# Kernel optimization log

Hardware: AMD Instinct MI355X
Metric: run time of the kernel (lower is better)

## Reference

```python
import jax, jax.numpy as jnp
import numpy as np

D_K = 64  # per-head dim; source hardcodes d_k for the 1/sqrt(d_k) scale


def setup_inputs() -> dict:
    key = jax.random.key(0)
    kq, kk, kv = jax.random.split(key, 3)
    shape = (4, 16, 2048, D_K)  # [B, H, S, d]
    return {
        "q_s": jax.random.normal(kq, shape, dtype=jnp.float32),
        "k_s": jax.random.normal(kk, shape, dtype=jnp.float32),
        "v_s": jax.random.normal(kv, shape, dtype=jnp.float32),
    }


def reference(q_s, k_s, v_s):
    # scores = Q K^T / sqrt(d_k)  -> [B, H, S, S] (full matrix, unfused, as in source)
    scale = 1.0 / jnp.sqrt(jnp.asarray(D_K, dtype=q_s.dtype))
    scores = jnp.einsum("bhqd,bhkd->bhqk", q_s, k_s) * scale
    attn = jax.nn.softmax(scores, axis=-1)
    # out = attn @ V -> [B, H, S, d]
    return jnp.einsum("bhqk,bhkd->bhqd", attn, v_s)
```

## Files before the change

kernel.cpp:

```cpp
#include <hip/hip_runtime.h>
#include <stdint.h>
#include <math.h>

#define S_LEN 2048
#define DIM   64
#define QBLK  128
#define KVBLK 64
#define NKV   (S_LEN / KVBLK)

typedef __attribute__((ext_vector_type(8))) short short8;
typedef __attribute__((ext_vector_type(4))) float f32x4;

static __device__ __forceinline__ unsigned short f2bf(float f) {
    union { float f; uint32_t u; } cv; cv.f = f;
    uint32_t u = cv.u;
    return (unsigned short)((u + 0x7fffu + ((u >> 16) & 1u)) >> 16);
}

static __device__ __forceinline__ void gload16(const void* g, void* l) {
    __builtin_amdgcn_global_load_lds(
        (const __attribute__((address_space(1))) unsigned int*)g,
        (__attribute__((address_space(3))) unsigned int*)l, 16, 0, 0);
}

static __device__ __forceinline__ float vmax3(float a, float b, float c) {
    float d;
    asm("v_max3_f32 %0, %1, %2, %3" : "=v"(d) : "v"(a), "v"(b), "v"(c));
    return d;
}

__global__ void cvt_k(const float* __restrict__ kp, unsigned short* __restrict__ kws) {
    const int idx = blockIdx.x * 256 + threadIdx.x;
    const int c   = idx & 7;
    const int s   = (idx >> 3) & (S_LEN - 1);
    const int bh  = idx >> 14;
    const float* src = kp + ((size_t)bh * S_LEN + s) * DIM + c * 8;
    const f32x4 a = *reinterpret_cast<const f32x4*>(src);
    const f32x4 b = *reinterpret_cast<const f32x4*>(src + 4);
    short8 t;
    t[0] = (short)f2bf(a[0]); t[1] = (short)f2bf(a[1]);
    t[2] = (short)f2bf(a[2]); t[3] = (short)f2bf(a[3]);
    t[4] = (short)f2bf(b[0]); t[5] = (short)f2bf(b[1]);
    t[6] = (short)f2bf(b[2]); t[7] = (short)f2bf(b[3]);
    unsigned short* dst = kws + ((size_t)bh * S_LEN + s) * DIM + (size_t)((c ^ (s & 7)) * 8);
    *reinterpret_cast<short8*>(dst) = t;
}

__global__ void cvt_v(const float* __restrict__ vp, unsigned short* __restrict__ vtws) {
    const int bh = blockIdx.x >> 5;
    const int t  = blockIdx.x & 31;
    const int tid = threadIdx.x;
    __shared__ unsigned short ldsT[DIM][72];

    const int i = tid >> 2;
    const int dbase = (tid & 3) * 16;
    const float* src = vp + ((size_t)bh * S_LEN + t * 64 + i) * DIM + dbase;
#pragma unroll
    for (int q4 = 0; q4 < 4; ++q4) {
        const f32x4 a = *reinterpret_cast<const f32x4*>(src + q4 * 4);
#pragma unroll
        for (int j = 0; j < 4; ++j) ldsT[dbase + q4 * 4 + j][i] = f2bf(a[j]);
    }
    __syncthreads();
#pragma unroll
    for (int hh = 0; hh < 2; ++hh) {
        const int slot = tid + hh * 256;
        const int d = slot >> 3, c_st = slot & 7;
        const int cl = c_st ^ (d & 7);
        short8 t8;
#pragma unroll
        for (int j = 0; j < 8; ++j) {
            const int p = cl * 8 + j;
            const int kap = (p & 32) | ((p & 16) >> 1) | ((p & 8) >> 1) | ((p & 4) << 2) | (p & 3);
            t8[j] = (short)ldsT[d][kap];
        }
        unsigned short* dst = vtws + ((size_t)bh * DIM + d) * S_LEN + t * 64 + c_st * 8;
        *reinterpret_cast<short8*>(dst) = t8;
    }
}

__global__ __launch_bounds__(256, 4)
void attn_fwd(const float* __restrict__ qp, const unsigned short* __restrict__ kws,
              const unsigned short* __restrict__ vtws, float* __restrict__ op) {
    const int lb = (blockIdx.x & 7) * 128 + (blockIdx.x >> 3);
    const int bh = lb >> 4;
    const int qb = lb & 15;
    const int tid  = threadIdx.x;
    const int wave = tid >> 6;
    const int lane = tid & 63;
    const int g = lane >> 4;
    const int r = lane & 15;

    __shared__ unsigned short klds[2][KVBLK * DIM];
    __shared__ unsigned short vlds[2][DIM * KVBLK];

    const float*          qg    = qp   + (size_t)bh * (S_LEN * DIM);
    const unsigned short* kbase = kws  + (size_t)bh * (S_LEN * DIM);
    const unsigned short* vbase = vtws + (size_t)bh * (S_LEN * DIM);
    float*                og    = op   + (size_t)bh * (S_LEN * DIM);

    const float qscale = 0.125f * 1.44269504088896340736f;
    const int q0 = qb * QBLK + wave * 32;
    short8 qfrag[2][2];
#pragma unroll
    for (int mt = 0; mt < 2; ++mt) {
        const float* qrow = qg + (size_t)(q0 + mt * 16 + r) * DIM;
#pragma unroll
        for (int ks = 0; ks < 2; ++ks) {
            const f32x4 a = *reinterpret_cast<const f32x4*>(qrow + ks * 32 + 8 * g);
            const f32x4 b = *reinterpret_cast<const f32x4*>(qrow + ks * 32 + 8 * g + 4);
            short8 t;
            t[0] = (short)f2bf(a[0] * qscale); t[1] = (short)f2bf(a[1] * qscale);
            t[2] = (short)f2bf(a[2] * qscale); t[3] = (short)f2bf(a[3] * qscale);
            t[4] = (short)f2bf(b[0] * qscale); t[5] = (short)f2bf(b[1] * qscale);
            t[6] = (short)f2bf(b[2] * qscale); t[7] = (short)f2bf(b[3] * qscale);
            qfrag[mt][ks] = t;
        }
    }

    int off[4][2];
#pragma unroll
    for (int nt = 0; nt < 4; ++nt)
#pragma unroll
        for (int ks = 0; ks < 2; ++ks)
            off[nt][ks] = (nt * 16 + r) * DIM + (((ks << 2) | g) ^ (r & 7)) * 8;

    f32x4 o[2][4];
    float m_run[2], l_part[2];
#pragma unroll
    for (int mt = 0; mt < 2; ++mt) {
#pragma unroll
        for (int nt = 0; nt < 4; ++nt) { f32x4 z = {0.f, 0.f, 0.f, 0.f}; o[mt][nt] = z; }
        m_run[mt] = -INFINITY; l_part[mt] = 0.0f;
    }

    const int srow = lane >> 3, schk = lane & 7;
    auto stage = [&](int t, int buf) {
        const int kv0 = t * KVBLK;
#pragma unroll
        for (int h = 0; h < 2; ++h) {
            const int row = wave * 16 + h * 8;
            gload16(kbase + (size_t)(kv0 + row + srow) * DIM + schk * 8,
                    &klds[buf][row * DIM]);
            gload16(vbase + (size_t)(row + srow) * S_LEN + kv0 + schk * 8,
                    &vlds[buf][row * DIM]);
        }
    };

    stage(0, 0);
    __syncthreads();
    int cur = 0;

    const f32x4 z4 = {0.f, 0.f, 0.f, 0.f};

    for (int t = 0; t < NKV; ++t) {
        if (t + 1 < NKV) stage(t + 1, cur ^ 1);

        const unsigned short* kl = &klds[cur][0];
        const unsigned short* vl = &vlds[cur][0];

        f32x4 st[2][4];
        __builtin_amdgcn_s_setprio(1);
#pragma unroll
        for (int nt = 0; nt < 4; ++nt) {
            const short8 kf0 = *reinterpret_cast<const short8*>(kl + off[nt][0]);
            const short8 kf1 = *reinterpret_cast<const short8*>(kl + off[nt][1]);
            st[0][nt] = __builtin_amdgcn_mfma_f32_16x16x32_bf16(kf0, qfrag[0][0], z4, 0, 0, 0);
            st[1][nt] = __builtin_amdgcn_mfma_f32_16x16x32_bf16(kf0, qfrag[1][0], z4, 0, 0, 0);
            st[0][nt] = __builtin_amdgcn_mfma_f32_16x16x32_bf16(kf1, qfrag[0][1], st[0][nt], 0, 0, 0);
            st[1][nt] = __builtin_amdgcn_mfma_f32_16x16x32_bf16(kf1, qfrag[1][1], st[1][nt], 0, 0, 0);
        }
        __builtin_amdgcn_s_setprio(0);

#pragma unroll
        for (int mt = 0; mt < 2; ++mt) {
            const f32x4 s0 = st[mt][0], s1 = st[mt][1], s2 = st[mt][2], s3 = st[mt][3];
            const float a0 = vmax3(s0[0], s0[1], s0[2]);
            const float a1 = vmax3(s0[3], s1[0], s1[1]);
            const float a2 = vmax3(s1[2], s1[3], s2[0]);
            const float a3 = vmax3(s2[1], s2[2], s2[3]);
            const float a4 = vmax3(s3[0], s3[1], s3[2]);
            const float lane_mx = fmaxf(vmax3(a0, a1, a2), vmax3(a3, a4, s3[3]));
            if (__any(lane_mx > m_run[mt] + 8.0f)) {
                float mx = fmaxf(lane_mx, __shfl_xor(lane_mx, 16));
                mx = fmaxf(mx, __shfl_xor(mx, 32));
                const float mnew = fmaxf(m_run[mt], mx);
                const float al = __builtin_amdgcn_exp2f(m_run[mt] - mnew);
                m_run[mt] = mnew;
                l_part[mt] *= al;
#pragma unroll
                for (int nt = 0; nt < 4; ++nt) {
                    f32x4 tt = o[mt][nt];
                    tt[0] *= al; tt[1] *= al; tt[2] *= al; tt[3] *= al;
                    o[mt][nt] = tt;
                }
            }
            const float mnow = m_run[mt];
            f32x4 p[4];
#pragma unroll
            for (int nt = 0; nt < 4; ++nt) {
                p[nt][0] = __builtin_amdgcn_exp2f(st[mt][nt][0] - mnow);
                p[nt][1] = __builtin_amdgcn_exp2f(st[mt][nt][1] - mnow);
                p[nt][2] = __builtin_amdgcn_exp2f(st[mt][nt][2] - mnow);
                p[nt][3] = __builtin_amdgcn_exp2f(st[mt][nt][3] - mnow);
            }
            l_part[mt] += ((p[0][0] + p[0][1]) + (p[0][2] + p[0][3]))
                        + ((p[1][0] + p[1][1]) + (p[1][2] + p[1][3]))
                        + ((p[2][0] + p[2][1]) + (p[2][2] + p[2][3]))
                        + ((p[3][0] + p[3][1]) + (p[3][2] + p[3][3]));
            short8 pfrag[2];
#pragma unroll
            for (int ks = 0; ks < 2; ++ks) {
                union { uint32_t u[4]; short8 v; } fr;
                asm("v_cvt_pk_bf16_f32 %0, %1, %2" : "=v"(fr.u[0])
                    : "v"(p[2*ks][0]),   "v"(p[2*ks][1]));
                asm("v_cvt_pk_bf16_f32 %0, %1, %2" : "=v"(fr.u[1])
                    : "v"(p[2*ks][2]),   "v"(p[2*ks][3]));
                asm("v_cvt_pk_bf16_f32 %0, %1, %2" : "=v"(fr.u[2])
                    : "v"(p[2*ks+1][0]), "v"(p[2*ks+1][1]));
                asm("v_cvt_pk_bf16_f32 %0, %1, %2" : "=v"(fr.u[3])
                    : "v"(p[2*ks+1][2]), "v"(p[2*ks+1][3]));
                pfrag[ks] = fr.v;
            }
            __builtin_amdgcn_s_setprio(1);
#pragma unroll
            for (int ntd = 0; ntd < 4; ++ntd) {
                const short8 vf0 = *reinterpret_cast<const short8*>(vl + off[ntd][0]);
                const short8 vf1 = *reinterpret_cast<const short8*>(vl + off[ntd][1]);
                o[mt][ntd] = __builtin_amdgcn_mfma_f32_16x16x32_bf16(vf0, pfrag[0], o[mt][ntd], 0, 0, 0);
                o[mt][ntd] = __builtin_amdgcn_mfma_f32_16x16x32_bf16(vf1, pfrag[1], o[mt][ntd], 0, 0, 0);
            }
            __builtin_amdgcn_s_setprio(0);
        }

        __syncthreads();
        cur ^= 1;
    }

#pragma unroll
    for (int mt = 0; mt < 2; ++mt) {
        float lfull = l_part[mt];
        lfull += __shfl_xor(lfull, 16);
        lfull += __shfl_xor(lfull, 32);
        const float inv = 1.0f / lfull;
        float* dst = og + (size_t)(q0 + mt * 16 + r) * DIM + 4 * g;
#pragma unroll
        for (int ntd = 0; ntd < 4; ++ntd) {
            f32x4 tt = o[mt][ntd];
            tt[0] *= inv; tt[1] *= inv; tt[2] *= inv; tt[3] *= inv;
            *reinterpret_cast<f32x4*>(dst + ntd * 16) = tt;
        }
    }
}

extern "C" void kernel_launch(void* const* d_in, const int* in_sizes, int n_in,
                              void* d_out, int out_size, void* d_ws, size_t ws_size,
                              hipStream_t stream) {
    const float* q = (const float*)d_in[0];
    const float* k = (const float*)d_in[1];
    const float* v = (const float*)d_in[2];
    float* out = (float*)d_out;
    unsigned short* kws  = (unsigned short*)d_ws;
    unsigned short* vtws = kws + (size_t)64 * S_LEN * DIM;
    cvt_k<<<dim3(64 * S_LEN * 8 / 256), 256, 0, stream>>>(k, kws);
    cvt_v<<<dim3(64 * (S_LEN / 64)), 256, 0, stream>>>(v, vtws);
    attn_fwd<<<dim3(1024), 256, 0, stream>>>(q, kws, vtws, out);
}
```

Measured before the change: 110.3 us.

## Software-pipeline QK^T of the next KV tile with softmax and PV of the current tile

Splits K and V staging and restructures the KV loop so the QK^T MFMAs for tile t+1 are issued alongside the softmax and PV work for tile t. Two score register sets are used in ping-pong, and the loop is unrolled by two to keep buffer indices static. K is staged one tile ahead, while V for the current tile is staged during the same step. The goal is to overlap exp/VALU softmax work with matrix-core work. The cost is roughly 32 more accumulator VGPRs per lane, which could reduce occupancy, and the setprio hints around QK^T are dropped.

```diff
diff --git a/kernel.cpp b/kernel.cpp
--- a/kernel.cpp
+++ b/kernel.cpp
@@ -135,46 +135,43 @@
     }
 
     const int srow = lane >> 3, schk = lane & 7;
-    auto stage = [&](int t, int buf) {
+    auto stageK = [&](int t, int buf) {
         const int kv0 = t * KVBLK;
 #pragma unroll
         for (int h = 0; h < 2; ++h) {
             const int row = wave * 16 + h * 8;
             gload16(kbase + (size_t)(kv0 + row + srow) * DIM + schk * 8,
                     &klds[buf][row * DIM]);
+        }
+    };
+    auto stageV = [&](int t, int buf) {
+        const int kv0 = t * KVBLK;
+#pragma unroll
+        for (int h = 0; h < 2; ++h) {
+            const int row = wave * 16 + h * 8;
             gload16(vbase + (size_t)(row + srow) * S_LEN + kv0 + schk * 8,
                     &vlds[buf][row * DIM]);
         }
     };
 
-    stage(0, 0);
-    __syncthreads();
-    int cur = 0;
-
     const f32x4 z4 = {0.f, 0.f, 0.f, 0.f};
 
-    for (int t = 0; t < NKV; ++t) {
-        if (t + 1 < NKV) stage(t + 1, cur ^ 1);
-
-        const unsigned short* kl = &klds[cur][0];
-        const unsigned short* vl = &vlds[cur][0];
-
-        f32x4 st[2][4];
-        __builtin_amdgcn_s_setprio(1);
+    auto qk = [&](f32x4 (&stC)[2][4], const unsigned short* kl) {
 #pragma unroll
         for (int nt = 0; nt < 4; ++nt) {
             const short8 kf0 = *reinterpret_cast<const short8*>(kl + off[nt][0]);
             const short8 kf1 = *reinterpret_cast<const short8*>(kl + off[nt][1]);
-            st[0][nt] = __builtin_amdgcn_mfma_f32_16x16x32_bf16(kf0, qfrag[0][0], z4, 0, 0, 0);
-            st[1][nt] = __builtin_amdgcn_mfma_f32_16x16x32_bf16(kf0, qfrag[1][0], z4, 0, 0, 0);
-            st[0][nt] = __builtin_amdgcn_mfma_f32_16x16x32_bf16(kf1, qfrag[0][1], st[0][nt], 0, 0, 0);
-            st[1][nt] = __builtin_amdgcn_mfma_f32_16x16x32_bf16(kf1, qfrag[1][1], st[1][nt], 0, 0, 0);
-        }
-        __builtin_amdgcn_s_setprio(0);
-
+            stC[0][nt] = __builtin_amdgcn_mfma_f32_16x16x32_bf16(kf0, qfrag[0][0], z4, 0, 0, 0);
+            stC[1][nt] = __builtin_amdgcn_mfma_f32_16x16x32_bf16(kf0, qfrag[1][0], z4, 0, 0, 0);
+            stC[0][nt] = __builtin_amdgcn_mfma_f32_16x16x32_bf16(kf1, qfrag[0][1], stC[0][nt], 0, 0, 0);
+            stC[1][nt] = __builtin_amdgcn_mfma_f32_16x16x32_bf16(kf1, qfrag[1][1], stC[1][nt], 0, 0, 0);
+        }
+    };
+
+    auto smpv = [&](f32x4 (&stP)[2][4], const unsigned short* vl) {
 #pragma unroll
         for (int mt = 0; mt < 2; ++mt) {
-            const f32x4 s0 = st[mt][0], s1 = st[mt][1], s2 = st[mt][2], s3 = st[mt][3];
+            const f32x4 s0 = stP[mt][0], s1 = stP[mt][1], s2 = stP[mt][2], s3 = stP[mt][3];
             const float a0 = vmax3(s0[0], s0[1], s0[2]);
             const float a1 = vmax3(s0[3], s1[0], s1[1]);
             const float a2 = vmax3(s1[2], s1[3], s2[0]);
@@ -199,10 +196,10 @@
             f32x4 p[4];
 #pragma unroll
             for (int nt = 0; nt < 4; ++nt) {
-                p[nt][0] = __builtin_amdgcn_exp2f(st[mt][nt][0] - mnow);
-                p[nt][1] = __builtin_amdgcn_exp2f(st[mt][nt][1] - mnow);
-                p[nt][2] = __builtin_amdgcn_exp2f(st[mt][nt][2] - mnow);
-                p[nt][3] = __builtin_amdgcn_exp2f(st[mt][nt][3] - mnow);
+                p[nt][0] = __builtin_amdgcn_exp2f(stP[mt][nt][0] - mnow);
+                p[nt][1] = __builtin_amdgcn_exp2f(stP[mt][nt][1] - mnow);
+                p[nt][2] = __builtin_amdgcn_exp2f(stP[mt][nt][2] - mnow);
+                p[nt][3] = __builtin_amdgcn_exp2f(stP[mt][nt][3] - mnow);
             }
             l_part[mt] += ((p[0][0] + p[0][1]) + (p[0][2] + p[0][3]))
                         + ((p[1][0] + p[1][1]) + (p[1][2] + p[1][3]))
@@ -232,10 +229,35 @@
             }
             __builtin_amdgcn_s_setprio(0);
         }
-
-        __syncthreads();
-        cur ^= 1;
-    }
+    };
+
+    f32x4 stA[2][4], stB[2][4];
+
+    stageK(0, 0); stageV(0, 0);
+    __syncthreads();
+    stageK(1, 1);
+    qk(stA, &klds[0][0]);
+    __syncthreads();
+
+    for (int tt = 1; tt < NKV; tt += 2) {
+        {
+            const int t = tt;
+            if (t + 1 < NKV) stageK(t + 1, 0);
+            stageV(t, 1);
+            qk(stB, &klds[1][0]);
+            smpv(stA, &vlds[0][0]);
+            __syncthreads();
+        }
+        if (tt + 1 < NKV) {
+            const int t = tt + 1;
+            stageK(t + 1, 1);
+            stageV(t, 0);
+            qk(stA, &klds[0][0]);
+            smpv(stB, &vlds[1][0]);
+            __syncthreads();
+        }
+    }
+    smpv(stB, &vlds[1][0]);
 
 #pragma unroll
     for (int mt = 0; mt < 2; ++mt) {
```

Result: slower. 274.1 us (+148.5%).

## Halve Q and KV tiles, stage V through registers into padded LDS

Applied to the files above, without the earlier changes.

The Q block drops from 128 to 64 rows, so each wave now owns 16 query rows instead of 32. The KV block drops from 64 to 32, the grid doubles to 2048 blocks, and launch bounds target 8 blocks per CU for higher occupancy. V tiles are no longer copied straight into LDS. They are loaded into registers and written into an LDS buffer padded to a row stride of 40 after compute, and the loader addresses the column chunks of the existing V layout. In exchange, each K/V tile is reused by half as many query rows, so global and L2 traffic per output roughly doubles, and there are twice as many barriers per row.

```diff
diff --git a/kernel.cpp b/kernel.cpp
--- a/kernel.cpp
+++ b/kernel.cpp
@@ -4,9 +4,10 @@
 
 #define S_LEN 2048
 #define DIM   64
-#define QBLK  128
-#define KVBLK 64
+#define QBLK  64
+#define KVBLK 32
 #define NKV   (S_LEN / KVBLK)
+#define VSTR  40
 
 typedef __attribute__((ext_vector_type(8))) short short8;
 typedef __attribute__((ext_vector_type(4))) float f32x4;
@@ -79,12 +80,12 @@
     }
 }
 
-__global__ __launch_bounds__(256, 4)
+__global__ __launch_bounds__(256, 8)
 void attn_fwd(const float* __restrict__ qp, const unsigned short* __restrict__ kws,
               const unsigned short* __restrict__ vtws, float* __restrict__ op) {
-    const int lb = (blockIdx.x & 7) * 128 + (blockIdx.x >> 3);
-    const int bh = lb >> 4;
-    const int qb = lb & 15;
+    const int lb = (blockIdx.x & 7) * 256 + (blockIdx.x >> 3);
+    const int bh = lb >> 5;
+    const int qb = lb & 31;
     const int tid  = threadIdx.x;
     const int wave = tid >> 6;
     const int lane = tid & 63;
@@ -92,7 +93,7 @@
     const int r = lane & 15;
 
     __shared__ unsigned short klds[2][KVBLK * DIM];
-    __shared__ unsigned short vlds[2][DIM * KVBLK];
+    __shared__ unsigned short vlds[2][DIM * VSTR];
 
     const float*          qg    = qp   + (size_t)bh * (S_LEN * DIM);
     const unsigned short* kbase = kws  + (size_t)bh * (S_LEN * DIM);
@@ -100,11 +101,10 @@
     float*                og    = op   + (size_t)bh * (S_LEN * DIM);
 
     const float qscale = 0.125f * 1.44269504088896340736f;
-    const int q0 = qb * QBLK + wave * 32;
-    short8 qfrag[2][2];
-#pragma unroll
-    for (int mt = 0; mt < 2; ++mt) {
-        const float* qrow = qg + (size_t)(q0 + mt * 16 + r) * DIM;
+    const int q0 = qb * QBLK + wave * 16;
+    short8 qfrag[2];
+    {
+        const float* qrow = qg + (size_t)(q0 + r) * DIM;
 #pragma unroll
         for (int ks = 0; ks < 2; ++ks) {
             const f32x4 a = *reinterpret_cast<const f32x4*>(qrow + ks * 32 + 8 * g);
@@ -114,142 +114,131 @@
             t[2] = (short)f2bf(a[2] * qscale); t[3] = (short)f2bf(a[3] * qscale);
             t[4] = (short)f2bf(b[0] * qscale); t[5] = (short)f2bf(b[1] * qscale);
             t[6] = (short)f2bf(b[2] * qscale); t[7] = (short)f2bf(b[3] * qscale);
-            qfrag[mt][ks] = t;
-        }
-    }
-
-    int off[4][2];
-#pragma unroll
-    for (int nt = 0; nt < 4; ++nt)
+            qfrag[ks] = t;
+        }
+    }
+
+    f32x4 o[4];
+#pragma unroll
+    for (int nt = 0; nt < 4; ++nt) { f32x4 z = {0.f, 0.f, 0.f, 0.f}; o[nt] = z; }
+    float m_run = -INFINITY, l_part = 0.0f;
+
+    const int srow = lane >> 3, schk = lane & 7;
+    auto stageK = [&](int t, int buf) {
+        gload16(kbase + (size_t)(t * KVBLK + wave * 8 + srow) * DIM + schk * 8,
+                &klds[buf][(wave * 8) * DIM]);
+    };
+    const int vd = tid >> 2, vc = tid & 3;
+    auto loadV = [&](int t) {
+        const int sc = ((4 * (t & 1) + vc) ^ (vd & 7));
+        return *reinterpret_cast<const short8*>(
+            vbase + (size_t)vd * S_LEN + (t >> 1) * 64 + sc * 8);
+    };
+    const int vwoff = vd * VSTR + vc * 8;
+
+    int koff[2][2], voff[4];
+#pragma unroll
+    for (int nt = 0; nt < 2; ++nt)
 #pragma unroll
         for (int ks = 0; ks < 2; ++ks)
-            off[nt][ks] = (nt * 16 + r) * DIM + (((ks << 2) | g) ^ (r & 7)) * 8;
-
-    f32x4 o[2][4];
-    float m_run[2], l_part[2];
-#pragma unroll
-    for (int mt = 0; mt < 2; ++mt) {
-#pragma unroll
-        for (int nt = 0; nt < 4; ++nt) { f32x4 z = {0.f, 0.f, 0.f, 0.f}; o[mt][nt] = z; }
-        m_run[mt] = -INFINITY; l_part[mt] = 0.0f;
-    }
-
-    const int srow = lane >> 3, schk = lane & 7;
-    auto stage = [&](int t, int buf) {
-        const int kv0 = t * KVBLK;
-#pragma unroll
-        for (int h = 0; h < 2; ++h) {
-            const int row = wave * 16 + h * 8;
-            gload16(kbase + (size_t)(kv0 + row + srow) * DIM + schk * 8,
-                    &klds[buf][row * DIM]);
-            gload16(vbase + (size_t)(row + srow) * S_LEN + kv0 + schk * 8,
-                    &vlds[buf][row * DIM]);
-        }
-    };
-
-    stage(0, 0);
+            koff[nt][ks] = (nt * 16 + r) * DIM + (((ks << 2) | g) ^ (r & 7)) * 8;
+#pragma unroll
+    for (int nt = 0; nt < 4; ++nt) voff[nt] = (nt * 16 + r) * VSTR + g * 8;
+
+    const f32x4 z4 = {0.f, 0.f, 0.f, 0.f};
+
+    stageK(0, 0);
+    {
+        short8 v0 = loadV(0);
+        *reinterpret_cast<short8*>(&vlds[0][vwoff]) = v0;
+    }
     __syncthreads();
     int cur = 0;
 
-    const f32x4 z4 = {0.f, 0.f, 0.f, 0.f};
-
     for (int t = 0; t < NKV; ++t) {
-        if (t + 1 < NKV) stage(t + 1, cur ^ 1);
+        short8 vnext;
+        if (t + 1 < NKV) {
+            stageK(t + 1, cur ^ 1);
+            vnext = loadV(t + 1);
+        }
 
         const unsigned short* kl = &klds[cur][0];
+        __builtin_amdgcn_s_setprio(1);
+        const short8 kf00 = *reinterpret_cast<const short8*>(kl + koff[0][0]);
+        const short8 kf01 = *reinterpret_cast<const short8*>(kl + koff[0][1]);
+        const short8 kf10 = *reinterpret_cast<const short8*>(kl + koff[1][0]);
+        const short8 kf11 = *reinterpret_cast<const short8*>(kl + koff[1][1]);
+        f32x4 st0 = __builtin_amdgcn_mfma_f32_16x16x32_bf16(kf00, qfrag[0], z4, 0, 0, 0);
+        f32x4 st1 = __builtin_amdgcn_mfma_f32_16x16x32_bf16(kf10, qfrag[0], z4, 0, 0, 0);
+        st0 = __builtin_amdgcn_mfma_f32_16x16x32_bf16(kf01, qfrag[1], st0, 0, 0, 0);
+        st1 = __builtin_amdgcn_mfma_f32_16x16x32_bf16(kf11, qfrag[1], st1, 0, 0, 0);
+        __builtin_amdgcn_s_setprio(0);
+
+        const float a0 = vmax3(st0[0], st0[1], st0[2]);
+        const float a1 = vmax3(st0[3], st1[0], st1[1]);
+        const float a2 = fmaxf(st1[2], st1[3]);
+        const float lane_mx = vmax3(a0, a1, a2);
+        if (__any(lane_mx > m_run + 8.0f)) {
+            float mx = fmaxf(lane_mx, __shfl_xor(lane_mx, 16));
+            mx = fmaxf(mx, __shfl_xor(mx, 32));
+            const float mnew = fmaxf(m_run, mx);
+            const float al = __builtin_amdgcn_exp2f(m_run - mnew);
+            m_run = mnew;
+            l_part *= al;
+#pragma unroll
+            for (int nt = 0; nt < 4; ++nt) {
+                f32x4 sc = o[nt];
+                sc[0] *= al; sc[1] *= al; sc[2] *= al; sc[3] *= al;
+                o[nt] = sc;
+            }
+        }
+        f32x4 p0, p1;
+        p0[0] = __builtin_amdgcn_exp2f(st0[0] - m_run);
+        p0[1] = __builtin_amdgcn_exp2f(st0[1] - m_run);
+        p0[2] = __builtin_amdgcn_exp2f(st0[2] - m_run);
+        p0[3] = __builtin_amdgcn_exp2f(st0[3] - m_run);
+        p1[0] = __builtin_amdgcn_exp2f(st1[0] - m_run);
+        p1[1] = __builtin_amdgcn_exp2f(st1[1] - m_run);
+        p1[2] = __builtin_amdgcn_exp2f(st1[2] - m_run);
+        p1[3] = __builtin_amdgcn_exp2f(st1[3] - m_run);
+        l_part += ((p0[0] + p0[1]) + (p0[2] + p0[3])) + ((p1[0] + p1[1]) + (p1[2] + p1[3]));
+
+        short8 pfrag;
+        {
+            union { uint32_t u[4]; short8 v; } fr;
+            asm("v_cvt_pk_bf16_f32 %0, %1, %2" : "=v"(fr.u[0]) : "v"(p0[0]), "v"(p0[1]));
+            asm("v_cvt_pk_bf16_f32 %0, %1, %2" : "=v"(fr.u[1]) : "v"(p0[2]), "v"(p0[3]));
+            asm("v_cvt_pk_bf16_f32 %0, %1, %2" : "=v"(fr.u[2]) : "v"(p1[0]), "v"(p1[1]));
+            asm("v_cvt_pk_bf16_f32 %0, %1, %2" : "=v"(fr.u[3]) : "v"(p1[2]), "v"(p1[3]));
+            pfrag = fr.v;
+        }
+
         const unsigned short* vl = &vlds[cur][0];
-
-        f32x4 st[2][4];
         __builtin_amdgcn_s_setprio(1);
 #pragma unroll
         for (int nt = 0; nt < 4; ++nt) {
-            const short8 kf0 = *reinterpret_cast<const short8*>(kl + off[nt][0]);
-            const short8 kf1 = *reinterpret_cast<const short8*>(kl + off[nt][1]);
-            st[0][nt] = __builtin_amdgcn_mfma_f32_16x16x32_bf16(kf0, qfrag[0][0], z4, 0, 0, 0);
-            st[1][nt] = __builtin_amdgcn_mfma_f32_16x16x32_bf16(kf0, qfrag[1][0], z4, 0, 0, 0);
-            st[0][nt] = __builtin_amdgcn_mfma_f32_16x16x32_bf16(kf1, qfrag[0][1], st[0][nt], 0, 0, 0);
-            st[1][nt] = __builtin_amdgcn_mfma_f32_16x16x32_bf16(kf1, qfrag[1][1], st[1][nt], 0, 0, 0);
+            const short8 vf = *reinterpret_cast<const short8*>(vl + voff[nt]);
+            o[nt] = __builtin_amdgcn_mfma_f32_16x16x32_bf16(vf, pfrag, o[nt], 0, 0, 0);
         }
         __builtin_amdgcn_s_setprio(0);
 
-#pragma unroll
-        for (int mt = 0; mt < 2; ++mt) {
-            const f32x4 s0 = st[mt][0], s1 = st[mt][1], s2 = st[mt][2], s3 = st[mt][3];
-            const float a0 = vmax3(s0[0], s0[1], s0[2]);
-            const float a1 = vmax3(s0[3], s1[0], s1[1]);
-            const float a2 = vmax3(s1[2], s1[3], s2[0]);
-            const float a3 = vmax3(s2[1], s2[2], s2[3]);
-            const float a4 = vmax3(s3[0], s3[1], s3[2]);
-            const float lane_mx = fmaxf(vmax3(a0, a1, a2), vmax3(a3, a4, s3[3]));
-            if (__any(lane_mx > m_run[mt] + 8.0f)) {
-                float mx = fmaxf(lane_mx, __shfl_xor(lane_mx, 16));
-                mx = fmaxf(mx, __shfl_xor(mx, 32));
-                const float mnew = fmaxf(m_run[mt], mx);
-                const float al = __builtin_amdgcn_exp2f(m_run[mt] - mnew);
-                m_run[mt] = mnew;
-                l_part[mt] *= al;
-#pragma unroll
-                for (int nt = 0; nt < 4; ++nt) {
-                    f32x4 tt = o[mt][nt];
-                    tt[0] *= al; tt[1] *= al; tt[2] *= al; tt[3] *= al;
-                    o[mt][nt] = tt;
-                }
-            }
-            const float mnow = m_run[mt];
-            f32x4 p[4];
-#pragma unroll
-            for (int nt = 0; nt < 4; ++nt) {
-                p[nt][0] = __builtin_amdgcn_exp2f(st[mt][nt][0] - mnow);
-                p[nt][1] = __builtin_amdgcn_exp2f(st[mt][nt][1] - mnow);
-                p[nt][2] = __builtin_amdgcn_exp2f(st[mt][nt][2] - mnow);
-                p[nt][3] = __builtin_amdgcn_exp2f(st[mt][nt][3] - mnow);
-            }
-            l_part[mt] += ((p[0][0] + p[0][1]) + (p[0][2] + p[0][3]))
-                        + ((p[1][0] + p[1][1]) + (p[1][2] + p[1][3]))
-                        + ((p[2][0] + p[2][1]) + (p[2][2] + p[2][3]))
-                        + ((p[3][0] + p[3][1]) + (p[3][2] + p[3][3]));
-            short8 pfrag[2];
-#pragma unroll
-            for (int ks = 0; ks < 2; ++ks) {
-                union { uint32_t u[4]; short8 v; } fr;
-                asm("v_cvt_pk_bf16_f32 %0, %1, %2" : "=v"(fr.u[0])
-                    : "v"(p[2*ks][0]),   "v"(p[2*ks][1]));
-                asm("v_cvt_pk_bf16_f32 %0, %1, %2" : "=v"(fr.u[1])
-                    : "v"(p[2*ks][2]),   "v"(p[2*ks][3]));
-                asm("v_cvt_pk_bf16_f32 %0, %1, %2" : "=v"(fr.u[2])
-                    : "v"(p[2*ks+1][0]), "v"(p[2*ks+1][1]));
-                asm("v_cvt_pk_bf16_f32 %0, %1, %2" : "=v"(fr.u[3])
-                    : "v"(p[2*ks+1][2]), "v"(p[2*ks+1][3]));
-                pfrag[ks] = fr.v;
-            }
-            __builtin_amdgcn_s_setprio(1);
-#pragma unroll
-            for (int ntd = 0; ntd < 4; ++ntd) {
-                const short8 vf0 = *reinterpret_cast<const short8*>(vl + off[ntd][0]);
-                const short8 vf1 = *reinterpret_cast<const short8*>(vl + off[ntd][1]);
-                o[mt][ntd] = __builtin_amdgcn_mfma_f32_16x16x32_bf16(vf0, pfrag[0], o[mt][ntd], 0, 0, 0);
-                o[mt][ntd] = __builtin_amdgcn_mfma_f32_16x16x32_bf16(vf1, pfrag[1], o[mt][ntd], 0, 0, 0);
-            }
-            __builtin_amdgcn_s_setprio(0);
-        }
+        if (t + 1 < NKV)
+            *reinterpret_cast<short8*>(&vlds[cur ^ 1][vwoff]) = vnext;
 
         __syncthreads();
         cur ^= 1;
     }
 
-#pragma unroll
-    for (int mt = 0; mt < 2; ++mt) {
-        float lfull = l_part[mt];
-        lfull += __shfl_xor(lfull, 16);
-        lfull += __shfl_xor(lfull, 32);
-        const float inv = 1.0f / lfull;
-        float* dst = og + (size_t)(q0 + mt * 16 + r) * DIM + 4 * g;
-#pragma unroll
-        for (int ntd = 0; ntd < 4; ++ntd) {
-            f32x4 tt = o[mt][ntd];
-            tt[0] *= inv; tt[1] *= inv; tt[2] *= inv; tt[3] *= inv;
-            *reinterpret_cast<f32x4*>(dst + ntd * 16) = tt;
-        }
+    float lfull = l_part;
+    lfull += __shfl_xor(lfull, 16);
+    lfull += __shfl_xor(lfull, 32);
+    const float inv = 1.0f / lfull;
+    float* dst = og + (size_t)(q0 + r) * DIM + 4 * g;
+#pragma unroll
+    for (int nt = 0; nt < 4; ++nt) {
+        f32x4 tt = o[nt];
+        tt[0] *= inv; tt[1] *= inv; tt[2] *= inv; tt[3] *= inv;
+        *reinterpret_cast<f32x4*>(dst + nt * 16) = tt;
     }
 }
 
@@ -264,5 +253,5 @@
     unsigned short* vtws = kws + (size_t)64 * S_LEN * DIM;
     cvt_k<<<dim3(64 * S_LEN * 8 / 256), 256, 0, stream>>>(k, kws);
     cvt_v<<<dim3(64 * (S_LEN / 64)), 256, 0, stream>>>(v, vtws);
-    attn_fwd<<<dim3(1024), 256, 0, stream>>>(q, kws, vtws, out);
-}
+    attn_fwd<<<dim3(2048), 256, 0, stream>>>(q, kws, vtws, out);
+}
```

After: 124.7 us. 1.13x slower.

## Merge K/V conversion kernels and fold running-max subtraction into MFMA accumulator

Applied to the files above, without the earlier changes.

Combines the separate K and V bf16 conversion kernels into one launch with a branch on block index, removing one kernel launch and its tail. In the attention loop, the QK^T MFMA accumulator is seeded with -m_run, so scores arrive already shifted by the running max. That drops the per-element subtraction on the common path that does not rescale, and the max update becomes an incremental add. It changes the numerics slightly (m_run starts at 0, threshold relative to shifted scores) and adds per-iteration vector setup for the seed values.

```diff
diff --git a/kernel.cpp b/kernel.cpp
--- a/kernel.cpp
+++ b/kernel.cpp
@@ -29,53 +29,55 @@
     return d;
 }
 
-__global__ void cvt_k(const float* __restrict__ kp, unsigned short* __restrict__ kws) {
-    const int idx = blockIdx.x * 256 + threadIdx.x;
-    const int c   = idx & 7;
-    const int s   = (idx >> 3) & (S_LEN - 1);
-    const int bh  = idx >> 14;
-    const float* src = kp + ((size_t)bh * S_LEN + s) * DIM + c * 8;
-    const f32x4 a = *reinterpret_cast<const f32x4*>(src);
-    const f32x4 b = *reinterpret_cast<const f32x4*>(src + 4);
-    short8 t;
-    t[0] = (short)f2bf(a[0]); t[1] = (short)f2bf(a[1]);
-    t[2] = (short)f2bf(a[2]); t[3] = (short)f2bf(a[3]);
-    t[4] = (short)f2bf(b[0]); t[5] = (short)f2bf(b[1]);
-    t[6] = (short)f2bf(b[2]); t[7] = (short)f2bf(b[3]);
-    unsigned short* dst = kws + ((size_t)bh * S_LEN + s) * DIM + (size_t)((c ^ (s & 7)) * 8);
-    *reinterpret_cast<short8*>(dst) = t;
-}
-
-__global__ void cvt_v(const float* __restrict__ vp, unsigned short* __restrict__ vtws) {
-    const int bh = blockIdx.x >> 5;
-    const int t  = blockIdx.x & 31;
+__global__ void cvt_kv(const float* __restrict__ kp, const float* __restrict__ vp,
+                       unsigned short* __restrict__ kws, unsigned short* __restrict__ vtws) {
     const int tid = threadIdx.x;
     __shared__ unsigned short ldsT[DIM][72];
 
-    const int i = tid >> 2;
-    const int dbase = (tid & 3) * 16;
-    const float* src = vp + ((size_t)bh * S_LEN + t * 64 + i) * DIM + dbase;
-#pragma unroll
-    for (int q4 = 0; q4 < 4; ++q4) {
-        const f32x4 a = *reinterpret_cast<const f32x4*>(src + q4 * 4);
-#pragma unroll
-        for (int j = 0; j < 4; ++j) ldsT[dbase + q4 * 4 + j][i] = f2bf(a[j]);
-    }
-    __syncthreads();
-#pragma unroll
-    for (int hh = 0; hh < 2; ++hh) {
-        const int slot = tid + hh * 256;
-        const int d = slot >> 3, c_st = slot & 7;
-        const int cl = c_st ^ (d & 7);
-        short8 t8;
-#pragma unroll
-        for (int j = 0; j < 8; ++j) {
-            const int p = cl * 8 + j;
-            const int kap = (p & 32) | ((p & 16) >> 1) | ((p & 8) >> 1) | ((p & 4) << 2) | (p & 3);
-            t8[j] = (short)ldsT[d][kap];
-        }
-        unsigned short* dst = vtws + ((size_t)bh * DIM + d) * S_LEN + t * 64 + c_st * 8;
-        *reinterpret_cast<short8*>(dst) = t8;
+    if (blockIdx.x < 4096) {
+        const int idx = blockIdx.x * 256 + tid;
+        const int c   = idx & 7;
+        const int s   = (idx >> 3) & (S_LEN - 1);
+        const int bh  = idx >> 14;
+        const float* src = kp + ((size_t)bh * S_LEN + s) * DIM + c * 8;
+        const f32x4 a = *reinterpret_cast<const f32x4*>(src);
+        const f32x4 b = *reinterpret_cast<const f32x4*>(src + 4);
+        short8 t;
+        t[0] = (short)f2bf(a[0]); t[1] = (short)f2bf(a[1]);
+        t[2] = (short)f2bf(a[2]); t[3] = (short)f2bf(a[3]);
+        t[4] = (short)f2bf(b[0]); t[5] = (short)f2bf(b[1]);
+        t[6] = (short)f2bf(b[2]); t[7] = (short)f2bf(b[3]);
+        unsigned short* dst = kws + ((size_t)bh * S_LEN + s) * DIM + (size_t)((c ^ (s & 7)) * 8);
+        *reinterpret_cast<short8*>(dst) = t;
+    } else {
+        const int b  = blockIdx.x - 4096;
+        const int bh = b >> 5;
+        const int T  = b & 31;
+        const int i = tid >> 2;
+        const int dbase = (tid & 3) * 16;
+        const float* src = vp + ((size_t)bh * S_LEN + T * 64 + i) * DIM + dbase;
+#pragma unroll
+        for (int q4 = 0; q4 < 4; ++q4) {
+            const f32x4 a = *reinterpret_cast<const f32x4*>(src + q4 * 4);
+#pragma unroll
+            for (int j = 0; j < 4; ++j) ldsT[dbase + q4 * 4 + j][i] = f2bf(a[j]);
+        }
+        __syncthreads();
+#pragma unroll
+        for (int hh = 0; hh < 2; ++hh) {
+            const int slot = tid + hh * 256;
+            const int d = slot >> 3, c_st = slot & 7;
+            const int cl = c_st ^ (d & 7);
+            short8 t8;
+#pragma unroll
+            for (int j = 0; j < 8; ++j) {
+                const int p = cl * 8 + j;
+                const int kap = (p & 32) | ((p & 16) >> 1) | ((p & 8) >> 1) | ((p & 4) << 2) | (p & 3);
+                t8[j] = (short)ldsT[d][kap];
+            }
+            unsigned short* dst = vtws + ((size_t)bh * DIM + d) * S_LEN + T * 64 + c_st * 8;
+            *reinterpret_cast<short8*>(dst) = t8;
+        }
     }
 }
 
@@ -118,20 +120,13 @@
         }
     }
 
-    int off[4][2];
-#pragma unroll
-    for (int nt = 0; nt < 4; ++nt)
-#pragma unroll
-        for (int ks = 0; ks < 2; ++ks)
-            off[nt][ks] = (nt * 16 + r) * DIM + (((ks << 2) | g) ^ (r & 7)) * 8;
-
     f32x4 o[2][4];
     float m_run[2], l_part[2];
 #pragma unroll
     for (int mt = 0; mt < 2; ++mt) {
 #pragma unroll
         for (int nt = 0; nt < 4; ++nt) { f32x4 z = {0.f, 0.f, 0.f, 0.f}; o[mt][nt] = z; }
-        m_run[mt] = -INFINITY; l_part[mt] = 0.0f;
+        m_run[mt] = 0.0f; l_part[mt] = 0.0f;
     }
 
     const int srow = lane >> 3, schk = lane & 7;
@@ -147,17 +142,26 @@
         }
     };
 
+    int off[4][2];
+#pragma unroll
+    for (int nt = 0; nt < 4; ++nt)
+#pragma unroll
+        for (int ks = 0; ks < 2; ++ks)
+            off[nt][ks] = (nt * 16 + r) * DIM + (((ks << 2) | g) ^ (r & 7)) * 8;
+
     stage(0, 0);
     __syncthreads();
     int cur = 0;
 
-    const f32x4 z4 = {0.f, 0.f, 0.f, 0.f};
-
     for (int t = 0; t < NKV; ++t) {
         if (t + 1 < NKV) stage(t + 1, cur ^ 1);
 
         const unsigned short* kl = &klds[cur][0];
         const unsigned short* vl = &vlds[cur][0];
+
+        f32x4 ms0, ms1;
+        ms0[0] = ms0[1] = ms0[2] = ms0[3] = -m_run[0];
+        ms1[0] = ms1[1] = ms1[2] = ms1[3] = -m_run[1];
 
         f32x4 st[2][4];
         __builtin_amdgcn_s_setprio(1);
@@ -165,8 +169,8 @@
         for (int nt = 0; nt < 4; ++nt) {
             const short8 kf0 = *reinterpret_cast<const short8*>(kl + off[nt][0]);
             const short8 kf1 = *reinterpret_cast<const short8*>(kl + off[nt][1]);
-            st[0][nt] = __builtin_amdgcn_mfma_f32_16x16x32_bf16(kf0, qfrag[0][0], z4, 0, 0, 0);
-            st[1][nt] = __builtin_amdgcn_mfma_f32_16x16x32_bf16(kf0, qfrag[1][0], z4, 0, 0, 0);
+            st[0][nt] = __builtin_amdgcn_mfma_f32_16x16x32_bf16(kf0, qfrag[0][0], ms0, 0, 0, 0);
+            st[1][nt] = __builtin_amdgcn_mfma_f32_16x16x32_bf16(kf0, qfrag[1][0], ms1, 0, 0, 0);
             st[0][nt] = __builtin_amdgcn_mfma_f32_16x16x32_bf16(kf1, qfrag[0][1], st[0][nt], 0, 0, 0);
             st[1][nt] = __builtin_amdgcn_mfma_f32_16x16x32_bf16(kf1, qfrag[1][1], st[1][nt], 0, 0, 0);
         }
@@ -181,45 +185,47 @@
             const float a3 = vmax3(s2[1], s2[2], s2[3]);
             const float a4 = vmax3(s3[0], s3[1], s3[2]);
             const float lane_mx = fmaxf(vmax3(a0, a1, a2), vmax3(a3, a4, s3[3]));
-            if (__any(lane_mx > m_run[mt] + 8.0f)) {
+            f32x4 p[4];
+            if (__any(lane_mx > 8.0f)) {
                 float mx = fmaxf(lane_mx, __shfl_xor(lane_mx, 16));
                 mx = fmaxf(mx, __shfl_xor(mx, 32));
-                const float mnew = fmaxf(m_run[mt], mx);
-                const float al = __builtin_amdgcn_exp2f(m_run[mt] - mnew);
-                m_run[mt] = mnew;
+                const float al = __builtin_amdgcn_exp2f(-mx);
+                m_run[mt] += mx;
                 l_part[mt] *= al;
 #pragma unroll
                 for (int nt = 0; nt < 4; ++nt) {
-                    f32x4 tt = o[mt][nt];
-                    tt[0] *= al; tt[1] *= al; tt[2] *= al; tt[3] *= al;
-                    o[mt][nt] = tt;
+                    f32x4 sc = o[mt][nt];
+                    sc[0] *= al; sc[1] *= al; sc[2] *= al; sc[3] *= al;
+                    o[mt][nt] = sc;
                 }
-            }
-            const float mnow = m_run[mt];
-            f32x4 p[4];
-#pragma unroll
-            for (int nt = 0; nt < 4; ++nt) {
-                p[nt][0] = __builtin_amdgcn_exp2f(st[mt][nt][0] - mnow);
-                p[nt][1] = __builtin_amdgcn_exp2f(st[mt][nt][1] - mnow);
-                p[nt][2] = __builtin_amdgcn_exp2f(st[mt][nt][2] - mnow);
-                p[nt][3] = __builtin_amdgcn_exp2f(st[mt][nt][3] - mnow);
-            }
-            l_part[mt] += ((p[0][0] + p[0][1]) + (p[0][2] + p[0][3]))
-                        + ((p[1][0] + p[1][1]) + (p[1][2] + p[1][3]))
-                        + ((p[2][0] + p[2][1]) + (p[2][2] + p[2][3]))
-                        + ((p[3][0] + p[3][1]) + (p[3][2] + p[3][3]));
+#pragma unroll
+                for (int nt = 0; nt < 4; ++nt) {
+                    p[nt][0] = __builtin_amdgcn_exp2f(st[mt][nt][0] - mx);
+                    p[nt][1] = __builtin_amdgcn_exp2f(st[mt][nt][1] - mx);
+                    p[nt][2] = __builtin_amdgcn_exp2f(st[mt][nt][2] - mx);
+                    p[nt][3] = __builtin_amdgcn_exp2f(st[mt][nt][3] - mx);
+                }
+            } else {
+#pragma unroll
+                for (int nt = 0; nt < 4; ++nt) {
+                    p[nt][0] = __builtin_amdgcn_exp2f(st[mt][nt][0]);
+                    p[nt][1] = __builtin_amdgcn_exp2f(st[mt][nt][1]);
+                    p[nt][2] = __builtin_amdgcn_exp2f(st[mt][nt][2]);
+                    p[nt][3] = __builtin_amdgcn_exp2f(st[mt][nt][3]);
+                }
+            }
+            l_part[mt] += (((p[0][0] + p[0][1]) + (p[0][2] + p[0][3]))
+                         + ((p[1][0] + p[1][1]) + (p[1][2] + p[1][3])))
+                        + (((p[2][0] + p[2][1]) + (p[2][2] + p[2][3]))
+                         + ((p[3][0] + p[3][1]) + (p[3][2] + p[3][3])));
             short8 pfrag[2];
 #pragma unroll
             for (int ks = 0; ks < 2; ++ks) {
                 union { uint32_t u[4]; short8 v; } fr;
-                asm("v_cvt_pk_bf16_f32 %0, %1, %2" : "=v"(fr.u[0])
-                    : "v"(p[2*ks][0]),   "v"(p[2*ks][1]));
-                asm("v_cvt_pk_bf16_f32 %0, %1, %2" : "=v"(fr.u[1])
-                    : "v"(p[2*ks][2]),   "v"(p[2*ks][3]));
-                asm("v_cvt_pk_bf16_f32 %0, %1, %2" : "=v"(fr.u[2])
-                    : "v"(p[2*ks+1][0]), "v"(p[2*ks+1][1]));
-                asm("v_cvt_pk_bf16_f32 %0, %1, %2" : "=v"(fr.u[3])
-                    : "v"(p[2*ks+1][2]), "v"(p[2*ks+1][3]));
+                asm("v_cvt_pk_bf16_f32 %0, %1, %2" : "=v"(fr.u[0]) : "v"(p[2*ks][0]),   "v"(p[2*ks][1]));
+                asm("v_cvt_pk_bf16_f32 %0, %1, %2" : "=v"(fr.u[1]) : "v"(p[2*ks][2]),   "v"(p[2*ks][3]));
+                asm("v_cvt_pk_bf16_f32 %0, %1, %2" : "=v"(fr.u[2]) : "v"(p[2*ks+1][0]), "v"(p[2*ks+1][1]));
+                asm("v_cvt_pk_bf16_f32 %0, %1, %2" : "=v"(fr.u[3]) : "v"(p[2*ks+1][2]), "v"(p[2*ks+1][3]));
                 pfrag[ks] = fr.v;
             }
             __builtin_amdgcn_s_setprio(1);
@@ -262,7 +268,6 @@
     float* out = (float*)d_out;
     unsigned short* kws  = (unsigned short*)d_ws;
     unsigned short* vtws = kws + (size_t)64 * S_LEN * DIM;
-    cvt_k<<<dim3(64 * S_LEN * 8 / 256), 256, 0, stream>>>(k, kws);
-    cvt_v<<<dim3(64 * (S_LEN / 64)), 256, 0, stream>>>(v, vtws);
+    cvt_kv<<<dim3(6144), 256, 0, stream>>>(k, v, kws, vtws);
     attn_fwd<<<dim3(1024), 256, 0, stream>>>(q, kws, vtws, out);
 }
```

Result: slower. 121.1 us (+9.8%).
